# Kernel tuning notes

Measured on AMD Instinct MI355X. Metric: run time of the kernel, lower is better.

Reference implementation:

```python
import jax, jax.numpy as jnp
import numpy as np

D_MODEL = 1024
D_STATE = 16
D_CONV = 4
EXPAND = 2
D_INNER = EXPAND * D_MODEL          # 2048
DT_RANK = (D_MODEL + 15) // 16      # 64
B_SZ, L = 2, 2048


def setup_inputs() -> dict:
    key = jax.random.key(0)
    ks = jax.random.split(key, 14)
    s = 0.02
    dt_init = jax.random.uniform(ks[10], (D_INNER,), minval=1e-3, maxval=0.1)
    A = jnp.tile(jnp.arange(1, D_STATE + 1, dtype=jnp.float32)[None, :], (D_INNER, 1))
    return {
        "x_f": jax.random.normal(ks[0], (B_SZ, L, D_MODEL), jnp.float32),
        "x_h": jax.random.normal(ks[1], (B_SZ, L, D_MODEL), jnp.float32),
        "W_hf": s * jax.random.normal(ks[2], (D_MODEL, D_MODEL), jnp.float32),
        "b_hf": jnp.zeros((D_MODEL,), jnp.float32),
        "W_in": s * jax.random.normal(ks[3], (2 * D_INNER, D_MODEL), jnp.float32),
        "conv_w": s * jax.random.normal(ks[4], (D_INNER, 1, D_CONV), jnp.float32),
        "conv_b": jnp.zeros((D_INNER,), jnp.float32),
        "W_x": s * jax.random.normal(ks[5], (DT_RANK + 2 * D_STATE, D_INNER), jnp.float32),
        "W_dt": (DT_RANK ** -0.5) * jax.random.normal(ks[6], (D_INNER, DT_RANK), jnp.float32),
        "b_dt": jnp.log(jnp.expm1(dt_init)),
        "A_log": jnp.log(A),
        "D": jnp.ones((D_INNER,), jnp.float32),
        "W_out": s * jax.random.normal(ks[7], (D_MODEL, D_INNER), jnp.float32),
    }


def _mamba(x, W_in, conv_w, conv_b, W_x, W_dt, b_dt, A_log, D, W_out):
    B, Lx, _ = x.shape
    # in_proj -> x, z branches  [B, L, 2*d_inner]
    xz = jnp.einsum("bld,ed->ble", x, W_in)
    x_in, z = jnp.split(xz, 2, axis=-1)
    # causal depthwise conv1d, kernel d_conv, groups = d_inner
    x_nch = jnp.transpose(x_in, (0, 2, 1))  # [B, d_inner, L]
    x_conv = jax.lax.conv_general_dilated(
        x_nch, conv_w, window_strides=(1,), padding=[(D_CONV - 1, 0)],
        dimension_numbers=("NCH", "OIH", "NCH"), feature_group_count=D_INNER)
    x_c = jax.nn.silu(jnp.transpose(x_conv, (0, 2, 1)) + conv_b)  # [B, L, d_inner]
    # input-dependent dt, B, C
    x_dbl = jnp.einsum("ble,fe->blf", x_c, W_x)
    dt_r = x_dbl[..., :DT_RANK]
    B_ssm = x_dbl[..., DT_RANK:DT_RANK + D_STATE]          # [B, L, d_state]
    C_ssm = x_dbl[..., DT_RANK + D_STATE:]                  # [B, L, d_state]
    dt = jax.nn.softplus(jnp.einsum("blr,er->ble", dt_r, W_dt) + b_dt)  # [B, L, d_inner]
    A = -jnp.exp(A_log)  # [d_inner, d_state]

    # selective scan over time; carry h: [B, d_inner, d_state]
    def step(h, inp):
        dt_t, B_t, C_t, x_t = inp  # [B,d_inner], [B,d_state], [B,d_state], [B,d_inner]
        dA = jnp.exp(dt_t[:, :, None] * A)                       # [B, d_inner, d_state]
        dBx = dt_t[:, :, None] * B_t[:, None, :] * x_t[:, :, None]
        h = dA * h + dBx
        y_t = jnp.einsum("bes,bs->be", h, C_t)
        return h, y_t

    seq = (jnp.transpose(dt, (1, 0, 2)), jnp.transpose(B_ssm, (1, 0, 2)),
           jnp.transpose(C_ssm, (1, 0, 2)), jnp.transpose(x_c, (1, 0, 2)))
    h0 = jnp.zeros((B, D_INNER, D_STATE), x.dtype)
    _, ys = jax.lax.scan(step, h0, seq)
    y = jnp.transpose(ys, (1, 0, 2)) + D * x_c   # skip term
    y = y * jax.nn.silu(z)                        # output gate
    return jnp.einsum("ble,de->bld", y, W_out)


def reference(x_f, x_h, W_hf, b_hf, W_in, conv_w, conv_b, W_x, W_dt, b_dt, A_log, D, W_out):
    hf_gate = jax.nn.sigmoid(jnp.einsum("bld,ed->ble", x_h, W_hf) + b_hf)
    modulated = x_f * hf_gate
    return _mamba(modulated, W_in, conv_w, conv_b, W_x, W_dt, b_dt, A_log, D, W_out)
```

## Files before the change

### kernel.cpp

```cpp
#include <hip/hip_runtime.h>
#include <hip/hip_bf16.h>
#include <math.h>

#define L_SEQ  2048
#define BATCH  2
#define DMODEL 1024
#define DINNER 2048
#define DSTATE 16
#define NCHUNK 64
#define LCH    (L_SEQ / NCHUNK)

typedef __attribute__((ext_vector_type(8))) short bf16x8;
typedef __attribute__((ext_vector_type(4))) float f32x4;

__device__ __forceinline__ unsigned short f2bu(float x) {
    __hip_bfloat16 h = __float2bfloat16(x);
    return __builtin_bit_cast(unsigned short, h);
}
__device__ __forceinline__ float bu2f(unsigned short u) {
    __hip_bfloat16 h = __builtin_bit_cast(__hip_bfloat16, u);
    return __bfloat162float(h);
}
__device__ __forceinline__ float fast_exp2(float x) {
    float r; asm("v_exp_f32 %0, %1" : "=v"(r) : "v"(x)); return r;
}
#define LOG2E 1.44269504088896f

__global__ __launch_bounds__(256) void cvt_all(
    const float* __restrict__ Wout, const float* __restrict__ Win,
    const float* __restrict__ xh,   const float* __restrict__ Whf,
    const float* __restrict__ Wx,   const float* __restrict__ Wdt,
    __hip_bfloat16* __restrict__ dWout, __hip_bfloat16* __restrict__ dWin,
    __hip_bfloat16* __restrict__ dxh,   __hip_bfloat16* __restrict__ dWhf,
    __hip_bfloat16* __restrict__ dWx,   __hip_bfloat16* __restrict__ dWdt)
{
    int bid = blockIdx.x;
    const float* s; __hip_bfloat16* d;
    if (bid < 2048)       { s = Wout; d = dWout; }
    else if (bid < 6144)  { s = Win;  d = dWin;  bid -= 2048; }
    else if (bid < 10240) { s = xh;   d = dxh;   bid -= 6144; }
    else if (bid < 11264) { s = Whf;  d = dWhf;  bid -= 10240; }
    else if (bid < 11520) {
        bid -= 11264;
        const int i = (bid * 256 + threadIdx.x) * 4;
        const int r = i >> 11;
        ushort4 u = {0, 0, 0, 0};
        if (r < 96) {
            const float4 v = *reinterpret_cast<const float4*>(&Wx[i]);
            u.x = f2bu(v.x); u.y = f2bu(v.y); u.z = f2bu(v.z); u.w = f2bu(v.w);
        }
        *reinterpret_cast<ushort4*>(&dWx[i]) = u;
        return;
    }
    else                  { s = Wdt;  d = dWdt;  bid -= 11520; }
    const int i = (bid * 256 + threadIdx.x) * 4;
    const float4 v = *reinterpret_cast<const float4*>(&s[i]);
    ushort4 u;
    u.x = f2bu(v.x); u.y = f2bu(v.y); u.z = f2bu(v.z); u.w = f2bu(v.w);
    *reinterpret_cast<ushort4*>(&d[i]) = u;
}

__global__ __launch_bounds__(512) void mfma_gemm256(
    const __hip_bfloat16* __restrict__ A,
    const __hip_bfloat16* __restrict__ Bw,
    __hip_bfloat16* __restrict__ Cb,
    __hip_bfloat16* __restrict__ Cb2)
{
    __shared__ unsigned short As[2][256 * 64];
    __shared__ unsigned short Bs[2][256 * 64];
    const int tid = threadIdx.x;
    const int row0 = blockIdx.y * 256;
    const int col0 = blockIdx.x * 256;
    const int wid = tid >> 6, lane = tid & 63;
    const int wr = wid >> 2, wc = wid & 3;
    const int fr = lane & 15, fq = lane >> 4;

    f32x4 acc[8][4];
#pragma unroll
    for (int m = 0; m < 8; m++)
#pragma unroll
        for (int n = 0; n < 4; n++) acc[m][n] = (f32x4){0.f, 0.f, 0.f, 0.f};

    size_t gA[4], gB[4];
    int ld0[4];
#pragma unroll
    for (int l = 0; l < 4; l++) {
        const int item = l * 512 + tid;
        const int r = item >> 3, sl = item & 7;
        const int slw = sl ^ (r & 7);
        gA[l] = (size_t)(row0 + r) * 1024 + slw * 8;
        gB[l] = (size_t)(col0 + r) * 1024 + slw * 8;
        ld0[l] = item * 8;
    }

#if __has_builtin(__builtin_amdgcn_global_load_lds)
    auto STAGE = [&](int buf, int koff) {
#pragma unroll
        for (int l = 0; l < 4; l++)
            __builtin_amdgcn_global_load_lds(
                (const __attribute__((address_space(1))) unsigned int*)(A + gA[l] + koff),
                (__attribute__((address_space(3))) unsigned int*)&As[buf][ld0[l]], 16, 0, 0);
#pragma unroll
        for (int l = 0; l < 4; l++)
            __builtin_amdgcn_global_load_lds(
                (const __attribute__((address_space(1))) unsigned int*)(Bw + gB[l] + koff),
                (__attribute__((address_space(3))) unsigned int*)&Bs[buf][ld0[l]], 16, 0, 0);
    };
#else
    auto STAGE = [&](int buf, int koff) {
#pragma unroll
        for (int l = 0; l < 4; l++) {
            *reinterpret_cast<uint4*>(&As[buf][ld0[l]]) =
                *reinterpret_cast<const uint4*>(A + gA[l] + koff);
            *reinterpret_cast<uint4*>(&Bs[buf][ld0[l]]) =
                *reinterpret_cast<const uint4*>(Bw + gB[l] + koff);
        }
    };
#endif

    STAGE(0, 0);
    __syncthreads();
    int buf = 0;
    const int swz = fr & 7;
    for (int t = 0; t < 16; t++) {
        if (t + 1 < 16) STAGE(buf ^ 1, (t + 1) * 64);
#pragma unroll
        for (int ks = 0; ks < 2; ks++) {
            bf16x8 a[8], b[4];
#pragma unroll
            for (int m = 0; m < 8; m++)
                a[m] = *reinterpret_cast<const bf16x8*>(
                    &As[buf][(wr * 128 + m * 16 + fr) * 64 +
                             (((ks * 4 + fq) ^ swz) * 8)]);
#pragma unroll
            for (int n = 0; n < 4; n++)
                b[n] = *reinterpret_cast<const bf16x8*>(
                    &Bs[buf][(wc * 64 + n * 16 + fr) * 64 +
                             (((ks * 4 + fq) ^ swz) * 8)]);
#pragma unroll
            for (int m = 0; m < 8; m++)
#pragma unroll
                for (int n = 0; n < 4; n++)
                    acc[m][n] = __builtin_amdgcn_mfma_f32_16x16x32_bf16(
                        a[m], b[n], acc[m][n], 0, 0, 0);
        }
        __syncthreads();
        buf ^= 1;
    }

    const int r0 = row0 + wr * 128;
    const int c0 = col0 + wc * 64;
    const bool isx = (col0 < 2048);
#pragma unroll
    for (int m = 0; m < 8; m++)
#pragma unroll
        for (int n = 0; n < 4; n++) {
            const int col = c0 + n * 16 + fr;
#pragma unroll
            for (int j = 0; j < 4; j++) {
                const int row = r0 + m * 16 + fq * 4 + j;
                const __hip_bfloat16 v = __float2bfloat16(acc[m][n][j]);
                if (isx) Cb[(size_t)row * 2048 + col] = v;
                else     Cb2[(size_t)row * 2048 + col - 2048] = v;
            }
        }
}

template <int EPI, bool SWAP>
__global__ __launch_bounds__(256) void mfma_gemm(
    const __hip_bfloat16* __restrict__ A, int lda,
    const __hip_bfloat16* __restrict__ Bw, int ldb,
    int ksz,
    float* __restrict__ Cf, int ldc,
    __hip_bfloat16* __restrict__ Cb,
    const float* __restrict__ bias,
    const float* __restrict__ mul, int ldmul)
{
    __shared__ unsigned short As[128 * 32];
    __shared__ unsigned short Bs[128 * 32];
    const int tid = threadIdx.x;
    const int by = SWAP ? blockIdx.x : blockIdx.y;
    const int bx = SWAP ? blockIdx.y : blockIdx.x;
    const int row0 = by * 128;
    const int col0 = bx * 128;
    const int wid = tid >> 6, lane = tid & 63;
    const int wr = wid >> 1, wc = wid & 1;
    const int fr = lane & 15, fq = lane >> 4;
    const int kz0 = blockIdx.z * ksz;

    f32x4 acc[4][4];
#pragma unroll
    for (int i = 0; i < 4; i++)
#pragma unroll
        for (int j = 0; j < 4; j++) acc[i][j] = (f32x4){0.f, 0.f, 0.f, 0.f};

    const int i0 = tid, i1 = tid + 256;
    const size_t ga0 = (size_t)(row0 + (i0 >> 2)) * lda + (i0 & 3) * 8;
    const size_t ga1 = (size_t)(row0 + (i1 >> 2)) * lda + (i1 & 3) * 8;
    const size_t gb0 = (size_t)(col0 + (i0 >> 2)) * ldb + (i0 & 3) * 8;
    const size_t gb1 = (size_t)(col0 + (i1 >> 2)) * ldb + (i1 & 3) * 8;
    const int nk = ksz >> 5;

    for (int kk = 0; kk < nk; kk++) {
        const int koff = kz0 + kk * 32;
#if __has_builtin(__builtin_amdgcn_global_load_lds)
        __syncthreads();
        __builtin_amdgcn_global_load_lds(
            (const __attribute__((address_space(1))) unsigned int*)(A + ga0 + koff),
            (__attribute__((address_space(3))) unsigned int*)&As[i0 * 8], 16, 0, 0);
        __builtin_amdgcn_global_load_lds(
            (const __attribute__((address_space(1))) unsigned int*)(A + ga1 + koff),
            (__attribute__((address_space(3))) unsigned int*)&As[i1 * 8], 16, 0, 0);
        __builtin_amdgcn_global_load_lds(
            (const __attribute__((address_space(1))) unsigned int*)(Bw + gb0 + koff),
            (__attribute__((address_space(3))) unsigned int*)&Bs[i0 * 8], 16, 0, 0);
        __builtin_amdgcn_global_load_lds(
            (const __attribute__((address_space(1))) unsigned int*)(Bw + gb1 + koff),
            (__attribute__((address_space(3))) unsigned int*)&Bs[i1 * 8], 16, 0, 0);
        __syncthreads();
#else
        const uint4 va0 = *reinterpret_cast<const uint4*>(A + ga0 + koff);
        const uint4 va1 = *reinterpret_cast<const uint4*>(A + ga1 + koff);
        const uint4 vb0 = *reinterpret_cast<const uint4*>(Bw + gb0 + koff);
        const uint4 vb1 = *reinterpret_cast<const uint4*>(Bw + gb1 + koff);
        __syncthreads();
        *reinterpret_cast<uint4*>(&As[i0 * 8]) = va0;
        *reinterpret_cast<uint4*>(&As[i1 * 8]) = va1;
        *reinterpret_cast<uint4*>(&Bs[i0 * 8]) = vb0;
        *reinterpret_cast<uint4*>(&Bs[i1 * 8]) = vb1;
        __syncthreads();
#endif
        bf16x8 af[4], bq[4];
#pragma unroll
        for (int rb = 0; rb < 4; rb++)
            af[rb] = *reinterpret_cast<const bf16x8*>(
                &As[(wr * 64 + rb * 16 + fr) * 32 + fq * 8]);
#pragma unroll
        for (int cb = 0; cb < 4; cb++)
            bq[cb] = *reinterpret_cast<const bf16x8*>(
                &Bs[(wc * 64 + cb * 16 + fr) * 32 + fq * 8]);
#pragma unroll
        for (int rb = 0; rb < 4; rb++)
#pragma unroll
            for (int cb = 0; cb < 4; cb++)
                acc[rb][cb] = __builtin_amdgcn_mfma_f32_16x16x32_bf16(
                    af[rb], bq[cb], acc[rb][cb], 0, 0, 0);
    }

    float* Cz = Cf;
    if (EPI == 0) {
        const int nrows = (SWAP ? gridDim.x : gridDim.y) * 128;
        Cz = Cf + (size_t)blockIdx.z * (size_t)nrows * ldc;
    }
    const int r0 = row0 + wr * 64, c0 = col0 + wc * 64;
#pragma unroll
    for (int rb = 0; rb < 4; rb++)
#pragma unroll
        for (int cb = 0; cb < 4; cb++) {
            const int col = c0 + cb * 16 + fr;
#pragma unroll
            for (int j = 0; j < 4; j++) {
                const int row = r0 + rb * 16 + fq * 4 + j;
                float v = acc[rb][cb][j];
                if (EPI == 0) {
                    Cz[(size_t)row * ldc + col] = v;
                } else if (EPI == 1) {
                    v = 1.f / (1.f + __expf(-(v + bias[col])));
                    v *= mul[(size_t)row * ldmul + col];
                    Cb[(size_t)row * ldc + col] = __float2bfloat16(v);
                } else {
                    v += bias[col];
                    v = (v > 20.f) ? v : log1pf(__expf(v));
                    Cb[(size_t)row * ldc + col] = __float2bfloat16(v);
                }
            }
        }
}

__global__ __launch_bounds__(256) void reduce_xdbl(
    const float* __restrict__ part, float* __restrict__ xdbl,
    __hip_bfloat16* __restrict__ dtr)
{
    const int i = blockIdx.x * 256 + threadIdx.x;
    float s = 0.f;
#pragma unroll
    for (int j = 0; j < 8; j++) s += part[(size_t)j * 524288 + i];
    xdbl[i] = s;
    const int col = i & 127;
    if (col < 64) dtr[((i >> 7) << 6) + col] = __float2bfloat16(s);
}

__global__ __launch_bounds__(256) void reduce_out(
    const float* __restrict__ part, float* __restrict__ out)
{
    const int i = (blockIdx.x * 256 + threadIdx.x) * 4;
    const float4 a = *reinterpret_cast<const float4*>(&part[i]);
    const float4 b = *reinterpret_cast<const float4*>(&part[4194304 + i]);
    *reinterpret_cast<float4*>(&out[i]) =
        make_float4(a.x + b.x, a.y + b.y, a.z + b.z, a.w + b.w);
}

__global__ __launch_bounds__(256) void conv_silu_kernel(
    const __hip_bfloat16* __restrict__ xin_b, const float* __restrict__ cw,
    const float* __restrict__ cb, __hip_bfloat16* __restrict__ xcb)
{
    int gid = blockIdx.x * 256 + threadIdx.x;
    int e = gid & (DINNER - 1);
    int row = gid >> 11;
    int t = row & (L_SEQ - 1);
    float s = cb[e];
#pragma unroll
    for (int j = 0; j < 4; j++) {
        int tt = t - 3 + j;
        if (tt >= 0)
            s = fmaf(cw[e * 4 + j],
                     __bfloat162float(xin_b[(size_t)(row - 3 + j) * 2048 + e]), s);
    }
    xcb[(size_t)row * 2048 + e] = __float2bfloat16(s / (1.f + __expf(-s)));
}

__global__ __launch_bounds__(256) void scan_pass_a(
    const __hip_bfloat16* __restrict__ dtb, const __hip_bfloat16* __restrict__ xcb,
    const float* __restrict__ xdbl, const float* __restrict__ A_log,
    __hip_bfloat16* __restrict__ hloc, __hip_bfloat16* __restrict__ Pp)
{
    __shared__ float sB[LCH][16];
    const int tid = threadIdx.x;
    const int e = (blockIdx.x << 8) + tid;
    const int chunk = blockIdx.y;
    const int b = blockIdx.z;
    const int t0 = chunk * LCH;

    if (tid < LCH * 4) {
        const int r = tid >> 2, sl = tid & 3;
        *(float4*)&sB[r][sl * 4] =
            *(const float4*)&xdbl[(size_t)(b * L_SEQ + t0 + r) * 128 + 64 + sl * 4];
    }
    float av[16];
#pragma unroll
    for (int sq = 0; sq < 4; sq++) {
        const float4 al = *(const float4*)&A_log[e * 16 + sq * 4];
#pragma unroll
        for (int j = 0; j < 4; j++)
            av[sq * 4 + j] = -fast_exp2(((const float*)&al)[j] * LOG2E);
    }
    float h[16];
#pragma unroll
    for (int s = 0; s < 16; s++) h[s] = 0.f;
    float sdt = 0.f;
    __syncthreads();

    const size_t rb = (size_t)(b * L_SEQ + t0) * 2048 + e;
    float dtv_n = __bfloat162float(dtb[rb]);
    float xv_n = __bfloat162float(xcb[rb]);
    for (int t = 0; t < LCH; t++) {
        const float dtv = dtv_n, xv = xv_n;
        if (t + 1 < LCH) {
            dtv_n = __bfloat162float(dtb[rb + (size_t)(t + 1) * 2048]);
            xv_n = __bfloat162float(xcb[rb + (size_t)(t + 1) * 2048]);
        }
        sdt += dtv;
        const float dtx = dtv * xv;
        const float dl2 = dtv * LOG2E;
#pragma unroll
        for (int sq = 0; sq < 4; sq++) {
            const float4 B4 = *(const float4*)&sB[t][sq * 4];
#pragma unroll
            for (int j = 0; j < 4; j++) {
                const int s = sq * 4 + j;
                const float Bv = ((const float*)&B4)[j];
                h[s] = fmaf(fast_exp2(dl2 * av[s]), h[s], Bv * dtx);
            }
        }
    }
    const size_t o = (((size_t)chunk * BATCH + b) * 2048 + e) * 16;
#pragma unroll
    for (int sq = 0; sq < 4; sq++) {
        ushort4 uh, up;
        uh.x = f2bu(h[sq * 4]);     uh.y = f2bu(h[sq * 4 + 1]);
        uh.z = f2bu(h[sq * 4 + 2]); uh.w = f2bu(h[sq * 4 + 3]);
        up.x = f2bu(fast_exp2(av[sq * 4] * sdt * LOG2E));
        up.y = f2bu(fast_exp2(av[sq * 4 + 1] * sdt * LOG2E));
        up.z = f2bu(fast_exp2(av[sq * 4 + 2] * sdt * LOG2E));
        up.w = f2bu(fast_exp2(av[sq * 4 + 3] * sdt * LOG2E));
        *(ushort4*)&hloc[o + sq * 4] = uh;
        *(ushort4*)&Pp[o + sq * 4] = up;
    }
}

__global__ __launch_bounds__(256) void scan_pass_b(
    const __hip_bfloat16* __restrict__ hloc, const __hip_bfloat16* __restrict__ Pp,
    __hip_bfloat16* __restrict__ h0)
{
    const int idx = blockIdx.x * 256 + threadIdx.x;
    float h = 0.f;
    h0[idx] = __float2bfloat16(0.f);
    for (int c = 0; c < NCHUNK - 1; c++) {
        const float P = __bfloat162float(Pp[(size_t)c * 65536 + idx]);
        const float hl = __bfloat162float(hloc[(size_t)c * 65536 + idx]);
        h = fmaf(P, h, hl);
        h0[(size_t)(c + 1) * 65536 + idx] = __float2bfloat16(h);
    }
}

__global__ __launch_bounds__(256) void scan_pass_c(
    const __hip_bfloat16* __restrict__ dtb, const __hip_bfloat16* __restrict__ xcb,
    const float* __restrict__ xdbl, const __hip_bfloat16* __restrict__ zb,
    const float* __restrict__ A_log, const float* __restrict__ Dw,
    const __hip_bfloat16* __restrict__ h0, __hip_bfloat16* __restrict__ yb)
{
    __shared__ float sB[LCH][16];
    __shared__ float sC[LCH][16];
    const int tid = threadIdx.x;
    const int e = (blockIdx.x << 8) + tid;
    const int chunk = blockIdx.y;
    const int b = blockIdx.z;
    const int t0 = chunk * LCH;

    if (tid < LCH * 4) {
        const int r = tid >> 2, sl = tid & 3;
        *(float4*)&sB[r][sl * 4] =
            *(const float4*)&xdbl[(size_t)(b * L_SEQ + t0 + r) * 128 + 64 + sl * 4];
    } else if (tid < LCH * 8) {
        const int t2 = tid - LCH * 4;
        const int r = t2 >> 2, sl = t2 & 3;
        *(float4*)&sC[r][sl * 4] =
            *(const float4*)&xdbl[(size_t)(b * L_SEQ + t0 + r) * 128 + 80 + sl * 4];
    }
    float av[16];
#pragma unroll
    for (int sq = 0; sq < 4; sq++) {
        const float4 al = *(const float4*)&A_log[e * 16 + sq * 4];
#pragma unroll
        for (int j = 0; j < 4; j++)
            av[sq * 4 + j] = -fast_exp2(((const float*)&al)[j] * LOG2E);
    }
    const float De = Dw[e];
    float h[16];
    const size_t o = (((size_t)chunk * BATCH + b) * 2048 + e) * 16;
#pragma unroll
    for (int sq = 0; sq < 4; sq++) {
        const ushort4 hv = *(const ushort4*)&h0[o + sq * 4];
        h[sq * 4]     = bu2f(hv.x); h[sq * 4 + 1] = bu2f(hv.y);
        h[sq * 4 + 2] = bu2f(hv.z); h[sq * 4 + 3] = bu2f(hv.w);
    }
    __syncthreads();

    const size_t rb = (size_t)(b * L_SEQ + t0) * 2048 + e;
    float dtv_n = __bfloat162float(dtb[rb]);
    float xv_n = __bfloat162float(xcb[rb]);
    float zv_n = __bfloat162float(zb[rb]);
    for (int t = 0; t < LCH; t++) {
        const float dtv = dtv_n, xv = xv_n, zv = zv_n;
        if (t + 1 < LCH) {
            dtv_n = __bfloat162float(dtb[rb + (size_t)(t + 1) * 2048]);
            xv_n = __bfloat162float(xcb[rb + (size_t)(t + 1) * 2048]);
            zv_n = __bfloat162float(zb[rb + (size_t)(t + 1) * 2048]);
        }
        const float dtx = dtv * xv;
        const float dl2 = dtv * LOG2E;
        float yp0 = 0.f, yp1 = 0.f, yp2 = 0.f, yp3 = 0.f;
#pragma unroll
        for (int sq = 0; sq < 4; sq++) {
            const float4 B4 = *(const float4*)&sB[t][sq * 4];
            const float4 C4 = *(const float4*)&sC[t][sq * 4];
#pragma unroll
            for (int j = 0; j < 4; j++) {
                const int s = sq * 4 + j;
                const float Bv = ((const float*)&B4)[j];
                const float Cv = ((const float*)&C4)[j];
                h[s] = fmaf(fast_exp2(dl2 * av[s]), h[s], Bv * dtx);
                if (sq == 0) yp0 = fmaf(h[s], Cv, yp0);
                else if (sq == 1) yp1 = fmaf(h[s], Cv, yp1);
                else if (sq == 2) yp2 = fmaf(h[s], Cv, yp2);
                else yp3 = fmaf(h[s], Cv, yp3);
            }
        }
        float yv = (yp0 + yp1) + (yp2 + yp3);
        yv = fmaf(De, xv, yv);
        const float sig = 1.f / (1.f + __expf(-zv));
        yb[rb + (size_t)t * 2048] = __float2bfloat16(yv * zv * sig);
    }
}

extern "C" void kernel_launch(void* const* d_in, const int* in_sizes, int n_in,
                              void* d_out, int out_size, void* d_ws, size_t ws_size,
                              hipStream_t stream)
{
    const float* x_f    = (const float*)d_in[0];
    const float* x_h    = (const float*)d_in[1];
    const float* W_hf   = (const float*)d_in[2];
    const float* b_hf   = (const float*)d_in[3];
    const float* W_in   = (const float*)d_in[4];
    const float* conv_w = (const float*)d_in[5];
    const float* conv_b = (const float*)d_in[6];
    const float* W_x    = (const float*)d_in[7];
    const float* W_dt   = (const float*)d_in[8];
    const float* b_dt   = (const float*)d_in[9];
    const float* A_log  = (const float*)d_in[10];
    const float* Dw     = (const float*)d_in[11];
    const float* W_out  = (const float*)d_in[12];
    float* out = (float*)d_out;
    float* ws  = (float*)d_ws;

    __hip_bfloat16* wout_b = (__hip_bfloat16*)(ws);
    __hip_bfloat16* win_b  = (__hip_bfloat16*)(ws + 1048576);
    __hip_bfloat16* xh_b   = (__hip_bfloat16*)(ws + 3145728);
    __hip_bfloat16* whf_b  = (__hip_bfloat16*)(ws + 5242880);
    __hip_bfloat16* m_b    = (__hip_bfloat16*)(ws + 5767168);
    __hip_bfloat16* hloc   = (__hip_bfloat16*)(ws + 1048576);
    __hip_bfloat16* Pp     = (__hip_bfloat16*)(ws + 3145728);
    __hip_bfloat16* h0     = (__hip_bfloat16*)(ws + 5242880);
    __hip_bfloat16* wx_b   = (__hip_bfloat16*)(ws + 7864320);
    __hip_bfloat16* wdt_b  = (__hip_bfloat16*)(ws + 7995392);
    __hip_bfloat16* dtr_b  = (__hip_bfloat16*)(ws + 8060928);
    float*          xdbl   = ws + 10289152;
    __hip_bfloat16* xin_b  = (__hip_bfloat16*)(ws + 10813440);
    __hip_bfloat16* z_b    = (__hip_bfloat16*)(ws + 15007744);
    __hip_bfloat16* xc_b   = (__hip_bfloat16*)(ws + 19202048);
    float*          part   = ws + 23396352;
    __hip_bfloat16* dt_b   = (__hip_bfloat16*)(ws + 27590656);
    float*          part7  = ws + 23396352;
    __hip_bfloat16* yb     = (__hip_bfloat16*)(ws + 31784960);

    cvt_all<<<11648, 256, 0, stream>>>(
        W_out, W_in, x_h, W_hf, W_x, W_dt,
        wout_b, win_b, xh_b, whf_b, wx_b, wdt_b);

    mfma_gemm<1, true><<<dim3(32, 8, 1), 256, 0, stream>>>(
        xh_b, DMODEL, whf_b, DMODEL, DMODEL,
        nullptr, DMODEL, m_b, b_hf, x_f, DMODEL);

    mfma_gemm256<<<dim3(16, 16, 1), 512, 0, stream>>>(
        m_b, win_b, xin_b, z_b);

    conv_silu_kernel<<<32768, 256, 0, stream>>>(
        xin_b, conv_w, conv_b, xc_b);

    mfma_gemm<0, false><<<dim3(1, 32, 8), 256, 0, stream>>>(
        xc_b, DINNER, wx_b, DINNER, 256,
        part, 128, nullptr, nullptr, nullptr, 0);
    reduce_xdbl<<<2048, 256, 0, stream>>>(part, xdbl, dtr_b);

    mfma_gemm<3, false><<<dim3(16, 32, 1), 256, 0, stream>>>(
        dtr_b, 64, wdt_b, 64, 64,
        nullptr, 2048, dt_b, b_dt, nullptr, 0);

    scan_pass_a<<<dim3(8, NCHUNK - 1, BATCH), 256, 0, stream>>>(
        dt_b, xc_b, xdbl, A_log, hloc, Pp);
    scan_pass_b<<<256, 256, 0, stream>>>(hloc, Pp, h0);
    scan_pass_c<<<dim3(8, NCHUNK, BATCH), 256, 0, stream>>>(
        dt_b, xc_b, xdbl, z_b, A_log, Dw, h0, yb);

    mfma_gemm<0, true><<<dim3(32, 8, 2), 256, 0, stream>>>(
        yb, DINNER, wout_b, DINNER, DINNER / 2,
        part7, DMODEL, nullptr, nullptr, nullptr, 0);
    reduce_out<<<4096, 256, 0, stream>>>(part7, out);
}
```

Baseline: 277.5 us.

## Use 256x256 split-K MFMA GEMM with bf16 partials for out_proj

```diff
diff --git a/kernel.cpp b/kernel.cpp
--- a/kernel.cpp
+++ b/kernel.cpp
@@ -60,9 +60,11 @@
     *reinterpret_cast<ushort4*>(&d[i]) = u;
 }
 
+template <int EPI>
 __global__ __launch_bounds__(512) void mfma_gemm256(
-    const __hip_bfloat16* __restrict__ A,
-    const __hip_bfloat16* __restrict__ Bw,
+    const __hip_bfloat16* __restrict__ A, int lda,
+    const __hip_bfloat16* __restrict__ Bw, int ldb,
+    int ksz,
     __hip_bfloat16* __restrict__ Cb,
     __hip_bfloat16* __restrict__ Cb2)
 {
@@ -74,6 +76,8 @@
     const int wid = tid >> 6, lane = tid & 63;
     const int wr = wid >> 2, wc = wid & 3;
     const int fr = lane & 15, fq = lane >> 4;
+    const int kz0 = blockIdx.z * ksz;
+    const int nk = ksz >> 6;
 
     f32x4 acc[8][4];
 #pragma unroll
@@ -88,8 +92,8 @@
         const int item = l * 512 + tid;
         const int r = item >> 3, sl = item & 7;
         const int slw = sl ^ (r & 7);
-        gA[l] = (size_t)(row0 + r) * 1024 + slw * 8;
-        gB[l] = (size_t)(col0 + r) * 1024 + slw * 8;
+        gA[l] = (size_t)(row0 + r) * lda + slw * 8;
+        gB[l] = (size_t)(col0 + r) * ldb + slw * 8;
         ld0[l] = item * 8;
     }
 
@@ -118,12 +122,12 @@
     };
 #endif
 
-    STAGE(0, 0);
+    STAGE(0, kz0);
     __syncthreads();
     int buf = 0;
     const int swz = fr & 7;
-    for (int t = 0; t < 16; t++) {
-        if (t + 1 < 16) STAGE(buf ^ 1, (t + 1) * 64);
+    for (int t = 0; t < nk; t++) {
+        if (t + 1 < nk) STAGE(buf ^ 1, kz0 + (t + 1) * 64);
 #pragma unroll
         for (int ks = 0; ks < 2; ks++) {
             bf16x8 a[8], b[4];
@@ -137,12 +141,14 @@
                 b[n] = *reinterpret_cast<const bf16x8*>(
                     &Bs[buf][(wc * 64 + n * 16 + fr) * 64 +
                              (((ks * 4 + fq) ^ swz) * 8)]);
+            __builtin_amdgcn_s_setprio(1);
 #pragma unroll
             for (int m = 0; m < 8; m++)
 #pragma unroll
                 for (int n = 0; n < 4; n++)
                     acc[m][n] = __builtin_amdgcn_mfma_f32_16x16x32_bf16(
                         a[m], b[n], acc[m][n], 0, 0, 0);
+            __builtin_amdgcn_s_setprio(0);
         }
         __syncthreads();
         buf ^= 1;
@@ -151,6 +157,9 @@
     const int r0 = row0 + wr * 128;
     const int c0 = col0 + wc * 64;
     const bool isx = (col0 < 2048);
+    const int ncols = gridDim.x * 256;
+    __hip_bfloat16* pz = Cb +
+        (size_t)blockIdx.z * (size_t)(gridDim.y * 256) * ncols;
 #pragma unroll
     for (int m = 0; m < 8; m++)
 #pragma unroll
@@ -160,8 +169,12 @@
             for (int j = 0; j < 4; j++) {
                 const int row = r0 + m * 16 + fq * 4 + j;
                 const __hip_bfloat16 v = __float2bfloat16(acc[m][n][j]);
-                if (isx) Cb[(size_t)row * 2048 + col] = v;
-                else     Cb2[(size_t)row * 2048 + col - 2048] = v;
+                if (EPI == 2) {
+                    if (isx) Cb[(size_t)row * 2048 + col] = v;
+                    else     Cb2[(size_t)row * 2048 + col - 2048] = v;
+                } else {
+                    pz[(size_t)row * ncols + col] = v;
+                }
             }
         }
 }
@@ -290,14 +303,18 @@
     if (col < 64) dtr[((i >> 7) << 6) + col] = __float2bfloat16(s);
 }
 
-__global__ __launch_bounds__(256) void reduce_out(
-    const float* __restrict__ part, float* __restrict__ out)
+__global__ __launch_bounds__(256) void reduce_out4(
+    const __hip_bfloat16* __restrict__ part, float* __restrict__ out)
 {
     const int i = (blockIdx.x * 256 + threadIdx.x) * 4;
-    const float4 a = *reinterpret_cast<const float4*>(&part[i]);
-    const float4 b = *reinterpret_cast<const float4*>(&part[4194304 + i]);
-    *reinterpret_cast<float4*>(&out[i]) =
-        make_float4(a.x + b.x, a.y + b.y, a.z + b.z, a.w + b.w);
+    float s0 = 0.f, s1 = 0.f, s2 = 0.f, s3 = 0.f;
+#pragma unroll
+    for (int z = 0; z < 4; z++) {
+        const ushort4 u = *reinterpret_cast<const ushort4*>(
+            &part[(size_t)z * 4194304 + i]);
+        s0 += bu2f(u.x); s1 += bu2f(u.y); s2 += bu2f(u.z); s3 += bu2f(u.w);
+    }
+    *reinterpret_cast<float4*>(&out[i]) = make_float4(s0, s1, s2, s3);
 }
 
 __global__ __launch_bounds__(256) void conv_silu_kernel(
@@ -520,7 +537,7 @@
     __hip_bfloat16* xc_b   = (__hip_bfloat16*)(ws + 19202048);
     float*          part   = ws + 23396352;
     __hip_bfloat16* dt_b   = (__hip_bfloat16*)(ws + 27590656);
-    float*          part7  = ws + 23396352;
+    __hip_bfloat16* part7b = (__hip_bfloat16*)(ws + 23396352);
     __hip_bfloat16* yb     = (__hip_bfloat16*)(ws + 31784960);
 
     cvt_all<<<11648, 256, 0, stream>>>(
@@ -531,8 +548,8 @@
         xh_b, DMODEL, whf_b, DMODEL, DMODEL,
         nullptr, DMODEL, m_b, b_hf, x_f, DMODEL);
 
-    mfma_gemm256<<<dim3(16, 16, 1), 512, 0, stream>>>(
-        m_b, win_b, xin_b, z_b);
+    mfma_gemm256<2><<<dim3(16, 16, 1), 512, 0, stream>>>(
+        m_b, DMODEL, win_b, DMODEL, DMODEL, xin_b, z_b);
 
     conv_silu_kernel<<<32768, 256, 0, stream>>>(
         xin_b, conv_w, conv_b, xc_b);
@@ -552,8 +569,7 @@
     scan_pass_c<<<dim3(8, NCHUNK, BATCH), 256, 0, stream>>>(
         dt_b, xc_b, xdbl, z_b, A_log, Dw, h0, yb);
 
-    mfma_gemm<0, true><<<dim3(32, 8, 2), 256, 0, stream>>>(
-        yb, DINNER, wout_b, DINNER, DINNER / 2,
-        part7, DMODEL, nullptr, nullptr, nullptr, 0);
-    reduce_out<<<4096, 256, 0, stream>>>(part7, out);
-}
+    mfma_gemm256<4><<<dim3(4, 16, 4), 512, 0, stream>>>(
+        yb, DINNER, wout_b, DINNER, DINNER / 4, part7b, nullptr);
+    reduce_out4<<<4096, 256, 0, stream>>>(part7b, out);
+}
```

Measured after the change: 273.8 us. About the same (-1.3%).
